# Kernel optimization log

Hardware: AMD Instinct MI355X
Metric: run time of the kernel (lower is better)

## Reference

```python
import jax, jax.numpy as jnp
import numpy as np

INTERVAL = 4
UPSCALE = 4
K = 3              # sample_size
SAMPLERS = 3
Q = 2 ** INTERVAL                 # 16
L = 2 ** (8 - INTERVAL) + 1       # 17
PAD = K - 1
B, H, W = 4, 512, 512

_STRIDES = np.array([L ** 3, L ** 2, L, 1], dtype=np.int32)


def ste_round(x):
    # straight-through round (round_func in the torch code)
    return x + jax.lax.stop_gradient(jnp.round(x) - x)


def fix_weight(w):
    return jnp.clip(ste_round(w * 127.0), -127.0, 127.0)


def sample(img, sw, sb):
    # unfold(K, K-1) + conv-per-patch + fold is exactly a VALID conv.
    # img: (B,1,h+PAD,w+PAD); sw: (4,1,K,K) -> a,b,c,d each (B,1,h,w)
    out = jax.lax.conv_general_dilated(img, sw, (1, 1), 'VALID',
        dimension_numbers=('NCHW', 'OIHW', 'NCHW')) + sb[None, :, None, None]
    return out[:, 0:1], out[:, 1:2], out[:, 2:3], out[:, 3:4]


def interp(lut, res_w, sw, sb, scale, img_in, prev_img):
    # InterpTorchBatch: 4D simplex interpolation into the quantized LUT.
    # Sorted-simplex form is equivalent to the 24-case masked torch code
    # (ties yield zero-weight terms, so tie ordering is irrelevant).
    w = fix_weight(lut)                                       # (L^4, scale*scale)
    a, b, c, d = sample(img_in, sw, sb)
    if prev_img is not None:
        rw = jnp.clip(res_w, 0.0, 1.0)
        pa, pb, pc, pd = sample(prev_img, sw, sb)
        a = rw[0, 0] * pa + (1.0 - rw[0, 0]) * a
        b = rw[0, 1] * pb + (1.0 - rw[0, 1]) * b
        c = rw[1, 0] * pc + (1.0 - rw[1, 0]) * c
        d = rw[1, 1] * pd + (1.0 - rw[1, 1]) * d
    vals = jnp.concatenate([a, b, c, d], axis=1).transpose(0, 2, 3, 1)   # (B,h,w,4)
    lo = jnp.floor_divide(vals, float(Q)).astype(jnp.int32)
    f = jnp.mod(vals, float(Q))
    order = jnp.argsort(-f, axis=-1)                          # fractional parts, descending
    fs = jnp.take_along_axis(f, order, axis=-1)
    strides = jnp.asarray(_STRIDES)
    base = jnp.sum(lo * strides, axis=-1)                     # flat index of p0000
    inc = jnp.cumsum(strides[order], axis=-1)
    verts = jnp.concatenate([base[..., None], base[..., None] + inc], axis=-1)  # (B,h,w,5)
    ws = jnp.concatenate([float(Q) - fs[..., :1], fs[..., :-1] - fs[..., 1:], fs[..., -1:]], axis=-1)
    p = w[verts]                                              # gather: (B,h,w,5,scale*scale)
    out = jnp.einsum('bhwv,bhwvk->bhwk', ws, p) / float(Q)
    bb, hh, ww, _ = out.shape
    out = out.reshape(bb, hh, ww, scale, scale).transpose(0, 1, 3, 2, 4)
    return out.reshape(bb, 1, hh * scale, ww * scale)


def _pad_rot(x, r):
    return jnp.pad(jnp.rot90(x, r, axes=(2, 3)),
                   ((0, 0), (0, 0), (0, PAD), (0, PAD)), mode='edge')


def rotate_input(lut, scale, sw, sb, x, res_w, prev_x):
    pred = jnp.zeros((), jnp.float32)
    for r in range(4):
        pr = None if prev_x is None else _pad_rot(prev_x, r)
        pred = pred + jnp.rot90(
            interp(lut, res_w, sw, sb, scale, _pad_rot(x, r), pr),
            (4 - r) % 4, axes=(2, 3))
        pred = ste_round(pred)
    return pred


def autolut_forward(x, lut0, lut1, samp0, samp1, sbias0, sbias1, resw1):
    x = x * 255.0
    # stage 0: scale 1, no residual, bias 127
    pred = 0.0
    for s in range(SAMPLERS):
        pred = pred + rotate_input(lut0[s], 1, samp0[s], sbias0[s], x, None, None)
    prev_x = x
    x = ste_round(jnp.clip(pred / (SAMPLERS * 4.0) + 127.0, 0.0, 255.0))
    # stage 1 (last): upscale, residual blend with previous stage input
    pred = 0.0
    for s in range(SAMPLERS):
        pred = pred + rotate_input(lut1[s], UPSCALE, samp1[s], sbias1[s], x, resw1[s], prev_x)
    x = ste_round(jnp.clip(pred / float(SAMPLERS), 0.0, 255.0))
    return x / 255.0   # phase == 'train'


def setup_inputs() -> dict:
    key = jax.random.key(0)
    ks = jax.random.split(key, 6)
    x = jax.random.uniform(ks[0], (B, 1, H, W), dtype=jnp.float32)
    lut0 = jax.random.uniform(ks[1], (SAMPLERS, L ** 4, 1), jnp.float32, -1.0, 1.0)
    lut1 = jax.random.uniform(ks[2], (SAMPLERS, L ** 4, UPSCALE * UPSCALE), jnp.float32, -1.0, 1.0)

    def mk_sampler(k):
        w = jax.random.normal(k, (SAMPLERS, 4, 1, K, K), dtype=jnp.float32)
        # convex combination of patch pixels -> sampled values stay in [0,255]
        return jax.nn.softmax(w.reshape(SAMPLERS, 4, -1), axis=-1).reshape(SAMPLERS, 4, 1, K, K)

    samp0 = mk_sampler(ks[3])
    samp1 = mk_sampler(ks[4])
    sbias0 = jnp.zeros((SAMPLERS, 4), jnp.float32)
    sbias1 = jnp.zeros((SAMPLERS, 4), jnp.float32)
    resw1 = jax.random.uniform(ks[5], (SAMPLERS, 2, 2), dtype=jnp.float32)
    return {"x": x, "lut0": lut0, "lut1": lut1, "samp0": samp0, "samp1": samp1,
            "sbias0": sbias0, "sbias1": sbias1, "resw1": resw1}


def reference(x, lut0, lut1, samp0, samp1, sbias0, sbias1, resw1):
    return autolut_forward(x, lut0, lut1, samp0, samp1, sbias0, sbias1, resw1)
```

## Files before the change

kernel.cpp:

```cpp
#include <hip/hip_runtime.h>
#include <math.h>

static constexpr int B_ = 4;
static constexpr int N_ = 512;
static constexpr int N4_ = 2048;
static constexpr int NPIX = B_ * N_ * N_;
static constexpr int LUT_ROWS = 83521;
static constexpr int SPAD = 83584;
static constexpr int ST0 = 4913, ST1 = 289, ST2 = 17, ST3 = 1;

__device__ __forceinline__ float fixw(float v) {
    v = rintf(v * 127.0f);
    return fminf(fmaxf(v, -127.0f), 127.0f);
}

__global__ void fix_lut0_kernel(const float* __restrict__ in, char* __restrict__ out) {
    int t = blockIdx.x * blockDim.x + threadIdx.x;
    int s = blockIdx.y;
    if (t < LUT_ROWS) out[(size_t)s * SPAD + t] = (char)(int)fixw(in[(size_t)s * LUT_ROWS + t]);
}

__global__ void fix_lut1_kernel(const float4* __restrict__ in, uchar4* __restrict__ out, int n4) {
    int t = blockIdx.x * blockDim.x + threadIdx.x;
    if (t < n4) {
        float4 v = in[t];
        uchar4 o;
        o.x = (unsigned char)((int)fixw(v.x) + 127);
        o.y = (unsigned char)((int)fixw(v.y) + 127);
        o.z = (unsigned char)((int)fixw(v.z) + 127);
        o.w = (unsigned char)((int)fixw(v.w) + 127);
        out[t] = o;
    }
}

struct Simplex {
    int v[5];
    float w[5];
};

__device__ __forceinline__ double pack_key(float f, unsigned stride) {
    unsigned long long u = ((unsigned long long)__float_as_uint(f) << 32) | stride;
    return __longlong_as_double((long long)u);
}
__device__ __forceinline__ float key_f(double k) {
    return __uint_as_float((unsigned)((unsigned long long)__double_as_longlong(k) >> 32));
}
__device__ __forceinline__ int key_s(double k) {
    return (int)(unsigned)__double_as_longlong(k);
}

__device__ __forceinline__ Simplex simplex4(float a, float b, float c, float d) {
    float fl0 = floorf(a * 0.0625f), fl1 = floorf(b * 0.0625f),
          fl2 = floorf(c * 0.0625f), fl3 = floorf(d * 0.0625f);
    float f0 = a - 16.0f * fl0, f1 = b - 16.0f * fl1,
          f2 = c - 16.0f * fl2, f3 = d - 16.0f * fl3;
    int l0 = min(max((int)fl0, 0), 15);
    int l1 = min(max((int)fl1, 0), 15);
    int l2 = min(max((int)fl2, 0), 15);
    int l3 = min(max((int)fl3, 0), 15);
    double k0 = pack_key(f0, (unsigned)ST0);
    double k1 = pack_key(f1, (unsigned)ST1);
    double k2 = pack_key(f2, (unsigned)ST2);
    double k3 = pack_key(f3, (unsigned)ST3);
#define CSWD(X, Y) { double mx_ = fmax(X, Y); Y = fmin(X, Y); X = mx_; }
    CSWD(k0, k1) CSWD(k2, k3) CSWD(k0, k2) CSWD(k1, k3) CSWD(k1, k2)
#undef CSWD
    Simplex s;
    s.v[0] = l0 * ST0 + l1 * ST1 + l2 * ST2 + l3;
    s.v[1] = s.v[0] + key_s(k0);
    s.v[2] = s.v[1] + key_s(k1);
    s.v[3] = s.v[2] + key_s(k2);
    s.v[4] = s.v[3] + key_s(k3);
    float g0 = key_f(k0), g1 = key_f(k1), g2 = key_f(k2), g3 = key_f(k3);
    s.w[0] = (16.0f - g0) * 0.0625f;
    s.w[1] = (g0 - g1) * 0.0625f;
    s.w[2] = (g1 - g2) * 0.0625f;
    s.w[3] = (g2 - g3) * 0.0625f;
    s.w[4] = g3 * 0.0625f;
    return s;
}

__device__ __forceinline__ bool tap_for_r(int r, int a, int c, int& di, int& dj) {
    if (r == 0) { di = a - 2; dj = c - 2; return (a >= 2) && (c >= 2); }
    if (r == 1) { di = 2 - c; dj = a - 2; return (a >= 2) && (c <= 2); }
    if (r == 2) { di = 2 - a; dj = 2 - c; return (a <= 2) && (c <= 2); }
    di = c - 2; dj = 2 - a; return (a <= 2) && (c >= 2);
}

__device__ __forceinline__ void acc4u(unsigned int q, float wv, float* oc) {
    oc[0] = fmaf(wv, (float)(q & 0xffu), oc[0]);
    oc[1] = fmaf(wv, (float)((q >> 8) & 0xffu), oc[1]);
    oc[2] = fmaf(wv, (float)((q >> 16) & 0xffu), oc[2]);
    oc[3] = fmaf(wv, (float)(q >> 24), oc[3]);
}

__global__ __launch_bounds__(1024, 4) void stage0_kernel(
    const float* __restrict__ x,
    const char* __restrict__ lut0q,
    const float* __restrict__ samp0,
    const float* __restrict__ sbias0,
    float* __restrict__ x1)
{
    __shared__ char luts[SPAD];

    int b    = blockIdx.x >> 8;
    int tile = blockIdx.x & 255;
    int i = ((tile >> 4) << 5) + (threadIdx.x >> 5);
    int j = ((tile & 15) << 5) + (threadIdx.x & 31);
    const float* xb = x + (size_t)b * N_ * N_;

    float vals[3][4][4];
    #pragma unroll
    for (int s = 0; s < 3; ++s)
        #pragma unroll
        for (int r = 0; r < 4; ++r)
            #pragma unroll
            for (int ch = 0; ch < 4; ++ch) vals[s][r][ch] = 0.0f;
    #pragma unroll
    for (int a = 0; a < 5; ++a) {
        int ri = min(max(i - 2 + a, 0), N_ - 1);
        const float* row = xb + ri * N_;
        #pragma unroll
        for (int c = 0; c < 5; ++c) {
            int ci = min(max(j - 2 + c, 0), N_ - 1);
            float px = row[ci] * 255.0f;
            #pragma unroll
            for (int r = 0; r < 4; ++r) {
                int di, dj;
                if (tap_for_r(r, a, c, di, dj)) {
                    #pragma unroll
                    for (int s = 0; s < 3; ++s)
                        #pragma unroll
                        for (int ch = 0; ch < 4; ++ch)
                            vals[s][r][ch] += samp0[s * 36 + ch * 9 + di * 3 + dj] * px;
                }
            }
        }
    }

    float pred = 0.0f;
    #pragma unroll
    for (int s = 0; s < 3; ++s) {
        __syncthreads();
        {
            const int4* src = (const int4*)(lut0q + (size_t)s * SPAD);
            int4* dst = (int4*)luts;
            for (int u = threadIdx.x; u < SPAD / 16; u += 1024) dst[u] = src[u];
        }
        __syncthreads();

        const float* sb = sbias0 + s * 4;
        float acc = 0.0f;
        #pragma unroll
        for (int r = 0; r < 4; ++r) {
            Simplex sx = simplex4(vals[s][r][0] + sb[0], vals[s][r][1] + sb[1],
                                  vals[s][r][2] + sb[2], vals[s][r][3] + sb[3]);
            float p0 = (float)luts[sx.v[0]];
            float p1 = (float)luts[sx.v[1]];
            float p2 = (float)luts[sx.v[2]];
            float p3 = (float)luts[sx.v[3]];
            float p4 = (float)luts[sx.v[4]];
            float o = sx.w[0] * p0 + sx.w[1] * p1 + sx.w[2] * p2
                    + sx.w[3] * p3 + sx.w[4] * p4;
            acc = rintf(acc + o);
        }
        pred += acc;
    }
    x1[(size_t)b * N_ * N_ + i * N_ + j] =
        rintf(fminf(fmaxf(pred / 12.0f + 127.0f, 0.0f), 255.0f));
}

__global__ __launch_bounds__(256) void stage1_kernel(
    const float* __restrict__ x,
    const float* __restrict__ x1,
    const unsigned char* __restrict__ lut1q,
    const float* __restrict__ samp1,
    const float* __restrict__ sbias1,
    const float* __restrict__ resw1,
    float* __restrict__ out)
{
    int b    = blockIdx.x >> 10;
    int tile = blockIdx.x & 1023;
    int i = ((tile >> 5) << 4) + (threadIdx.x >> 4);
    int j = ((tile & 31) << 4) + (threadIdx.x & 15);
    const float* xb  = x  + (size_t)b * N_ * N_;
    const float* x1b = x1 + (size_t)b * N_ * N_;

    float rw[3][4];
    #pragma unroll
    for (int s = 0; s < 3; ++s)
        #pragma unroll
        for (int ch = 0; ch < 4; ++ch)
            rw[s][ch] = fminf(fmaxf(resw1[s * 4 + ch], 0.0f), 1.0f);

    float vals[3][4][4];
    #pragma unroll
    for (int s = 0; s < 3; ++s)
        #pragma unroll
        for (int r = 0; r < 4; ++r)
            #pragma unroll
            for (int ch = 0; ch < 4; ++ch) vals[s][r][ch] = sbias1[s * 4 + ch];

    #pragma unroll
    for (int a = 0; a < 5; ++a) {
        int ri = min(max(i - 2 + a, 0), N_ - 1);
        const float* r1 = x1b + ri * N_;
        const float* r0 = xb + ri * N_;
        #pragma unroll
        for (int c = 0; c < 5; ++c) {
            int ci = min(max(j - 2 + c, 0), N_ - 1);
            float pc = r1[ci];
            float pp = r0[ci] * 255.0f;
            float dq = pp - pc;
            float q[3][4];
            #pragma unroll
            for (int s = 0; s < 3; ++s)
                #pragma unroll
                for (int ch = 0; ch < 4; ++ch)
                    q[s][ch] = fmaf(rw[s][ch], dq, pc);
            #pragma unroll
            for (int r = 0; r < 4; ++r) {
                int di, dj;
                if (tap_for_r(r, a, c, di, dj)) {
                    #pragma unroll
                    for (int s = 0; s < 3; ++s)
                        #pragma unroll
                        for (int ch = 0; ch < 4; ++ch)
                            vals[s][r][ch] += samp1[s * 36 + ch * 9 + di * 3 + dj] * q[s][ch];
                }
            }
        }
    }

    float tot[16];
    #pragma unroll
    for (int k = 0; k < 16; ++k) tot[k] = 0.0f;

    #pragma unroll
    for (int s = 0; s < 3; ++s) {
        const unsigned char* lut = lut1q + (size_t)s * LUT_ROWS * 16;

        float acc[16];
        #pragma unroll
        for (int k = 0; k < 16; ++k) acc[k] = 0.0f;

        #pragma unroll
        for (int r = 0; r < 4; ++r) {
            Simplex sx = simplex4(vals[s][r][0], vals[s][r][1], vals[s][r][2], vals[s][r][3]);
            float oc[16];
            #pragma unroll
            for (int k = 0; k < 16; ++k) oc[k] = 0.0f;
            #pragma unroll
            for (int v = 0; v < 5; ++v) {
                const uint4 q = *(const uint4*)(lut + (size_t)sx.v[v] * 16);
                float wv = sx.w[v];
                acc4u(q.x, wv, oc);
                acc4u(q.y, wv, oc + 4);
                acc4u(q.z, wv, oc + 8);
                acc4u(q.w, wv, oc + 12);
            }
            float S = sx.w[0] + sx.w[1] + sx.w[2] + sx.w[3] + sx.w[4];
            float bias = 127.0f * S;
            #pragma unroll
            for (int k = 0; k < 16; ++k) oc[k] -= bias;
            #pragma unroll
            for (int u = 0; u < 4; ++u)
                #pragma unroll
                for (int v2 = 0; v2 < 4; ++v2) {
                    int k = 4 * u + v2;
                    int c = (r == 0) ? (4 * u + v2)
                          : (r == 1) ? (4 * (3 - v2) + u)
                          : (r == 2) ? (4 * (3 - u) + (3 - v2))
                                     : (4 * v2 + (3 - u));
                    acc[k] = rintf(acc[k] + oc[c]);
                }
        }
        #pragma unroll
        for (int k = 0; k < 16; ++k) tot[k] += acc[k];
    }

    float* ob = out + (size_t)b * N4_ * N4_ + (size_t)(i * 4) * N4_ + (j * 4);
    #pragma unroll
    for (int u = 0; u < 4; ++u) {
        float4 val;
        val.x = rintf(fminf(fmaxf(tot[4 * u + 0] / 3.0f, 0.0f), 255.0f)) * (1.0f / 255.0f);
        val.y = rintf(fminf(fmaxf(tot[4 * u + 1] / 3.0f, 0.0f), 255.0f)) * (1.0f / 255.0f);
        val.z = rintf(fminf(fmaxf(tot[4 * u + 2] / 3.0f, 0.0f), 255.0f)) * (1.0f / 255.0f);
        val.w = rintf(fminf(fmaxf(tot[4 * u + 3] / 3.0f, 0.0f), 255.0f)) * (1.0f / 255.0f);
        *(float4*)(ob + (size_t)u * N4_) = val;
    }
}

extern "C" void kernel_launch(void* const* d_in, const int* in_sizes, int n_in,
                              void* d_out, int out_size, void* d_ws, size_t ws_size,
                              hipStream_t stream) {
    const float* x      = (const float*)d_in[0];
    const float* lut0   = (const float*)d_in[1];
    const float* lut1   = (const float*)d_in[2];
    const float* samp0  = (const float*)d_in[3];
    const float* samp1  = (const float*)d_in[4];
    const float* sbias0 = (const float*)d_in[5];
    const float* sbias1 = (const float*)d_in[6];
    const float* resw1  = (const float*)d_in[7];
    float* out = (float*)d_out;
    char* ws   = (char*)d_ws;

    const int N_L1 = 3 * LUT_ROWS * 16;
    size_t off_x1 = 0;
    size_t off_l0 = (size_t)NPIX * sizeof(float);
    size_t off_l1 = (off_l0 + (size_t)3 * SPAD + 15) & ~(size_t)15;

    float* x1 = (float*)(ws + off_x1);
    char* l0q = ws + off_l0;
    unsigned char* l1q = (unsigned char*)(ws + off_l1);

    const int threads = 256;

    dim3 g0((LUT_ROWS + threads - 1) / threads, 3);
    fix_lut0_kernel<<<g0, threads, 0, stream>>>(lut0, l0q);
    fix_lut1_kernel<<<(N_L1 / 4 + threads - 1) / threads, threads, 0, stream>>>(
        (const float4*)lut1, (uchar4*)l1q, N_L1 / 4);
    stage0_kernel<<<NPIX / 1024, 1024, 0, stream>>>(x, l0q, samp0, sbias0, x1);
    stage1_kernel<<<NPIX / threads, threads, 0, stream>>>(x, x1, l1q, samp1, sbias1, resw1, out);
}
```

Measured before the change: 294.0 us.

## Stage input halo tile in shared memory and compute sampler values per LUT

Stage1 now loads a 20x20 halo tile of (x1, 255*x - x1) pairs into shared memory once per block, replacing 25 per-thread global loads of each input. The sampling convolution is also moved inside the per-sampler loop, so only 16 sampled values are live at a time instead of 48. That cuts register pressure and could raise occupancy. In exchange it adds a __syncthreads and repeats the shared-memory reads for each of the three samplers.

```diff
diff --git a/kernel.cpp b/kernel.cpp
--- a/kernel.cpp
+++ b/kernel.cpp
@@ -179,66 +179,69 @@
     const float* __restrict__ resw1,
     float* __restrict__ out)
 {
+    __shared__ float2 pix[20 * 20];
+
     int b    = blockIdx.x >> 10;
     int tile = blockIdx.x & 1023;
-    int i = ((tile >> 5) << 4) + (threadIdx.x >> 4);
-    int j = ((tile & 31) << 4) + (threadIdx.x & 15);
+    int ti0 = (tile >> 5) << 4;
+    int tj0 = (tile & 31) << 4;
     const float* xb  = x  + (size_t)b * N_ * N_;
     const float* x1b = x1 + (size_t)b * N_ * N_;
 
-    float rw[3][4];
-    #pragma unroll
-    for (int s = 0; s < 3; ++s)
+    for (int u = threadIdx.x; u < 400; u += 256) {
+        int pi = u / 20, pj = u - pi * 20;
+        int gi = min(max(ti0 + pi - 2, 0), N_ - 1);
+        int gj = min(max(tj0 + pj - 2, 0), N_ - 1);
+        float pc = x1b[gi * N_ + gj];
+        float pp = xb[gi * N_ + gj] * 255.0f;
+        pix[u] = make_float2(pc, pp - pc);
+    }
+    __syncthreads();
+
+    int i = ti0 + (threadIdx.x >> 4);
+    int j = tj0 + (threadIdx.x & 15);
+    (void)i; (void)j;
+    const float2* pb = pix + (threadIdx.x >> 4) * 20 + (threadIdx.x & 15);
+
+    float tot[16];
+    #pragma unroll
+    for (int k = 0; k < 16; ++k) tot[k] = 0.0f;
+
+    #pragma unroll
+    for (int s = 0; s < 3; ++s) {
+        const float* w  = samp1 + s * 36;
+        const unsigned char* lut = lut1q + (size_t)s * LUT_ROWS * 16;
+        float rws[4];
         #pragma unroll
         for (int ch = 0; ch < 4; ++ch)
-            rw[s][ch] = fminf(fmaxf(resw1[s * 4 + ch], 0.0f), 1.0f);
-
-    float vals[3][4][4];
-    #pragma unroll
-    for (int s = 0; s < 3; ++s)
+            rws[ch] = fminf(fmaxf(resw1[s * 4 + ch], 0.0f), 1.0f);
+
+        float vals[4][4];
         #pragma unroll
         for (int r = 0; r < 4; ++r)
             #pragma unroll
-            for (int ch = 0; ch < 4; ++ch) vals[s][r][ch] = sbias1[s * 4 + ch];
-
-    #pragma unroll
-    for (int a = 0; a < 5; ++a) {
-        int ri = min(max(i - 2 + a, 0), N_ - 1);
-        const float* r1 = x1b + ri * N_;
-        const float* r0 = xb + ri * N_;
-        #pragma unroll
-        for (int c = 0; c < 5; ++c) {
-            int ci = min(max(j - 2 + c, 0), N_ - 1);
-            float pc = r1[ci];
-            float pp = r0[ci] * 255.0f;
-            float dq = pp - pc;
-            float q[3][4];
-            #pragma unroll
-            for (int s = 0; s < 3; ++s)
+            for (int ch = 0; ch < 4; ++ch) vals[r][ch] = sbias1[s * 4 + ch];
+
+        #pragma unroll
+        for (int a = 0; a < 5; ++a) {
+            #pragma unroll
+            for (int c = 0; c < 5; ++c) {
+                float2 P = pb[a * 20 + c];
+                float q[4];
                 #pragma unroll
                 for (int ch = 0; ch < 4; ++ch)
-                    q[s][ch] = fmaf(rw[s][ch], dq, pc);
-            #pragma unroll
-            for (int r = 0; r < 4; ++r) {
-                int di, dj;
-                if (tap_for_r(r, a, c, di, dj)) {
-                    #pragma unroll
-                    for (int s = 0; s < 3; ++s)
+                    q[ch] = fmaf(rws[ch], P.y, P.x);
+                #pragma unroll
+                for (int r = 0; r < 4; ++r) {
+                    int di, dj;
+                    if (tap_for_r(r, a, c, di, dj)) {
                         #pragma unroll
                         for (int ch = 0; ch < 4; ++ch)
-                            vals[s][r][ch] += samp1[s * 36 + ch * 9 + di * 3 + dj] * q[s][ch];
+                            vals[r][ch] += w[ch * 9 + di * 3 + dj] * q[ch];
+                    }
                 }
             }
         }
-    }
-
-    float tot[16];
-    #pragma unroll
-    for (int k = 0; k < 16; ++k) tot[k] = 0.0f;
-
-    #pragma unroll
-    for (int s = 0; s < 3; ++s) {
-        const unsigned char* lut = lut1q + (size_t)s * LUT_ROWS * 16;
 
         float acc[16];
         #pragma unroll
@@ -246,7 +249,7 @@
 
         #pragma unroll
         for (int r = 0; r < 4; ++r) {
-            Simplex sx = simplex4(vals[s][r][0], vals[s][r][1], vals[s][r][2], vals[s][r][3]);
+            Simplex sx = simplex4(vals[r][0], vals[r][1], vals[r][2], vals[r][3]);
             float oc[16];
             #pragma unroll
             for (int k = 0; k < 16; ++k) oc[k] = 0.0f;
@@ -279,7 +282,9 @@
         for (int k = 0; k < 16; ++k) tot[k] += acc[k];
     }
 
-    float* ob = out + (size_t)b * N4_ * N4_ + (size_t)(i * 4) * N4_ + (j * 4);
+    float* ob = out + (size_t)b * N4_ * N4_
+              + (size_t)((ti0 + (threadIdx.x >> 4)) * 4) * N4_
+              + ((tj0 + (threadIdx.x & 15)) * 4);
     #pragma unroll
     for (int u = 0; u < 4; ++u) {
         float4 val;
```

After: 287.3 us. 1.02x faster.
